# Kernel optimization log

Hardware: AMD Instinct MI355X
Metric: run time of the kernel (lower is better)

The kernel has to match this reference:

```python
import jax, jax.numpy as jnp
import numpy as np

SMOOTH_COEF = 0.025
FLOOR = 1e-06
B, T, C = 64, 4096, 128


def setup_inputs() -> dict:
    key = jax.random.key(0)
    k1, = jax.random.split(key, 1)
    inputs = jax.random.uniform(k1, (B, T, C), dtype=jnp.float32)  # nonneg spectrogram-like
    alpha = jnp.full((C,), 0.98, dtype=jnp.float32)
    delta = jnp.full((C,), 2.0, dtype=jnp.float32)
    root = jnp.full((C,), 2.0, dtype=jnp.float32)
    return {"inputs": inputs, "alpha": alpha, "delta": delta, "root": root}


def _ema(x, s):
    # m_t = s*x_t + (1-s)*m_{t-1}, with h_{-1} = x_0 => m_0 = x_0.
    # Linear recurrence via associative scan: pairs (a_t, b_t), m_t = a_t*m_{t-1} + b_t.
    Bn, Tn, Cn = x.shape
    a = jnp.full((Tn,), 1.0 - s, dtype=x.dtype).at[0].set(0.0)
    a = jnp.broadcast_to(a[None, :, None], x.shape)
    b = (s * x).at[:, 0, :].set(x[:, 0, :])

    def comb(c1, c2):
        a1, b1 = c1
        a2, b2 = c2
        return (a1 * a2, a2 * b1 + b2)

    _, m = jax.lax.associative_scan(comb, (a, b), axis=1)
    return m


def reference(inputs, alpha, delta, root):
    alpha_c = jnp.minimum(alpha, 1.0)          # [C]
    root_c = jnp.maximum(root, 1.0)            # [C]
    m = _ema(inputs, SMOOTH_COEF)              # [B,T,C] EMA smoother
    one_over_root = 1.0 / root_c
    term1 = jnp.power(FLOOR + m, alpha_c)
    term2 = jnp.power(inputs / term1 + delta, one_over_root)
    term3 = jnp.power(delta, one_over_root)
    return term2 - term3
```

## Files before the change

### kernel.cpp

```cpp
#include <hip/hip_runtime.h>


constexpr int Bn = 64, Tn = 4096, Cn = 128;
constexpr int NC = 256;
constexpr int Lc = Tn / NC;
constexpr int SUPER = 8;
constexpr int NSUP = NC / SUPER;
constexpr int SWIN = 4;
constexpr float SC  = 0.025f;
constexpr float OMS = 1.0f - SC;
constexpr float FLOORV = 1e-6f;

typedef float v4f __attribute__((ext_vector_type(4)));

__host__ __device__ constexpr float powN(float a, int n) {
    float r = 1.0f;
    for (int i = 0; i < n; ++i) r *= a;
    return r;
}
constexpr float ACH  = powN(OMS, Lc);
constexpr float ACHS = powN(OMS, Lc * SUPER);


__global__ __launch_bounds__(256) void k_partial(const float* __restrict__ x,
                                                 float* __restrict__ endv,
                                                 float* __restrict__ supv) {
    int gid   = blockIdx.x * 256 + threadIdx.x;
    int cg    = gid & 31;
    int chunk = (gid >> 5) & (NC - 1);
    int b     = gid >> 13;
    int sub   = threadIdx.x >> 5;

    const float4* xp = (const float4*)x + (size_t)(b * Tn + chunk * Lc) * (Cn / 4) + cg;

    float4 v = xp[0];
    float4 m;
    if (chunk == 0) {
        m = v;
    } else {
        m.x = SC * v.x; m.y = SC * v.y; m.z = SC * v.z; m.w = SC * v.w;
    }
#pragma unroll
    for (int t = 1; t < Lc; ++t) {
        v = xp[(size_t)t * (Cn / 4)];
        m.x = fmaf(OMS, m.x, SC * v.x);
        m.y = fmaf(OMS, m.y, SC * v.y);
        m.z = fmaf(OMS, m.z, SC * v.z);
        m.w = fmaf(OMS, m.w, SC * v.w);
    }
    ((float4*)endv)[(size_t)(b * NC + chunk) * (Cn / 4) + cg] = m;

    __shared__ float4 lds[SUPER][32];
    lds[sub][cg] = m;
    __syncthreads();
    if (threadIdx.x < 32) {
        float4 acc = lds[0][threadIdx.x];
#pragma unroll
        for (int i = 1; i < SUPER; ++i) {
            float4 e = lds[i][threadIdx.x];
            acc.x = fmaf(ACH, acc.x, e.x);
            acc.y = fmaf(ACH, acc.y, e.y);
            acc.z = fmaf(ACH, acc.z, e.z);
            acc.w = fmaf(ACH, acc.w, e.w);
        }
        ((float4*)supv)[(size_t)blockIdx.x * 32 + threadIdx.x] = acc;
    }
}

__device__ __forceinline__ float pcen_elem(float x, float m, float al, float dl,
                                           float oor, float t3) {
    float lg   = __builtin_amdgcn_logf(FLOORV + m);
    float inv1 = __builtin_amdgcn_exp2f(-al * lg);
    float base = fmaf(x, inv1, dl);
    return __builtin_amdgcn_exp2f(oor * __builtin_amdgcn_logf(base)) - t3;
}

__global__ __launch_bounds__(256) void k_final(const float* __restrict__ x,
                                               const float* __restrict__ alpha,
                                               const float* __restrict__ delta,
                                               const float* __restrict__ root,
                                               const float* __restrict__ endv,
                                               const float* __restrict__ supv,
                                               float* __restrict__ out) {
    int gid   = blockIdx.x * 256 + threadIdx.x;
    int cg    = gid & 31;
    int chunk = (gid >> 5) & (NC - 1);
    int b     = gid >> 13;

    int sc = chunk >> 3;
    const float4* Ep = (const float4*)supv + (size_t)b * NSUP * 32 + cg;
    const float4* ep = (const float4*)endv + (size_t)b * NC * (Cn / 4) + cg;

    float4 acc = {0.f, 0.f, 0.f, 0.f};
    int s0 = sc - SWIN; if (s0 < 0) s0 = 0;
#pragma unroll 4
    for (int s = s0; s < sc; ++s) {
        float4 E = Ep[(size_t)s * 32];
        acc.x = fmaf(ACHS, acc.x, E.x);
        acc.y = fmaf(ACHS, acc.y, E.y);
        acc.z = fmaf(ACHS, acc.z, E.z);
        acc.w = fmaf(ACHS, acc.w, E.w);
    }
#pragma unroll 7
    for (int j = sc * SUPER; j < chunk; ++j) {
        float4 e = ep[(size_t)j * (Cn / 4)];
        acc.x = fmaf(ACH, acc.x, e.x);
        acc.y = fmaf(ACH, acc.y, e.y);
        acc.z = fmaf(ACH, acc.z, e.z);
        acc.w = fmaf(ACH, acc.w, e.w);
    }

    int c0 = cg * 4;
    float4 al = *(const float4*)(alpha + c0);
    float4 dl = *(const float4*)(delta + c0);
    float4 rt = *(const float4*)(root + c0);
    al.x = fminf(al.x, 1.f); al.y = fminf(al.y, 1.f); al.z = fminf(al.z, 1.f); al.w = fminf(al.w, 1.f);
    rt.x = fmaxf(rt.x, 1.f); rt.y = fmaxf(rt.y, 1.f); rt.z = fmaxf(rt.z, 1.f); rt.w = fmaxf(rt.w, 1.f);
    float4 oor = {1.f / rt.x, 1.f / rt.y, 1.f / rt.z, 1.f / rt.w};
    float4 t3  = {exp2f(oor.x * log2f(dl.x)), exp2f(oor.y * log2f(dl.y)),
                  exp2f(oor.z * log2f(dl.z)), exp2f(oor.w * log2f(dl.w))};

    size_t xoff = (size_t)(b * Tn + chunk * Lc) * (Cn / 4) + cg;
    const float4* xp = (const float4*)x + xoff;
    v4f*          op = (v4f*)out + xoff;

    float4 v = xp[0];
    float4 m;
    if (chunk == 0) {
        m = v;
    } else {
        m.x = fmaf(OMS, acc.x, SC * v.x);
        m.y = fmaf(OMS, acc.y, SC * v.y);
        m.z = fmaf(OMS, acc.z, SC * v.z);
        m.w = fmaf(OMS, acc.w, SC * v.w);
    }
    v4f o;
    o.x = pcen_elem(v.x, m.x, al.x, dl.x, oor.x, t3.x);
    o.y = pcen_elem(v.y, m.y, al.y, dl.y, oor.y, t3.y);
    o.z = pcen_elem(v.z, m.z, al.z, dl.z, oor.z, t3.z);
    o.w = pcen_elem(v.w, m.w, al.w, dl.w, oor.w, t3.w);
    __builtin_nontemporal_store(o, op);

#pragma unroll
    for (int t = 1; t < Lc; ++t) {
        v = xp[(size_t)t * (Cn / 4)];
        m.x = fmaf(OMS, m.x, SC * v.x);
        m.y = fmaf(OMS, m.y, SC * v.y);
        m.z = fmaf(OMS, m.z, SC * v.z);
        m.w = fmaf(OMS, m.w, SC * v.w);
        o.x = pcen_elem(v.x, m.x, al.x, dl.x, oor.x, t3.x);
        o.y = pcen_elem(v.y, m.y, al.y, dl.y, oor.y, t3.y);
        o.z = pcen_elem(v.z, m.z, al.z, dl.z, oor.z, t3.z);
        o.w = pcen_elem(v.w, m.w, al.w, dl.w, oor.w, t3.w);
        __builtin_nontemporal_store(o, op + (size_t)t * (Cn / 4));
    }
}

extern "C" void kernel_launch(void* const* d_in, const int* in_sizes, int n_in,
                              void* d_out, int out_size, void* d_ws, size_t ws_size,
                              hipStream_t stream) {
    const float* x     = (const float*)d_in[0];
    const float* alpha = (const float*)d_in[1];
    const float* delta = (const float*)d_in[2];
    const float* root  = (const float*)d_in[3];
    float* out  = (float*)d_out;
    float* endv = (float*)d_ws;
    float* supv = (float*)d_ws + (size_t)Bn * NC * Cn;

    const int total = Bn * NC * (Cn / 4);
    k_partial<<<total / 256, 256, 0, stream>>>(x, endv, supv);
    k_final<<<total / 256, 256, 0, stream>>>(x, alpha, delta, root, endv, supv, out);
}
```

Baseline: 256.1 us.

## Fuse two-pass EMA scan into single kernel with decoupled look-back flags

Merges the partial-sum kernel and the final kernel into one. Each block keeps its 16 timesteps of input in registers, publishes its superchunk carry with an atomic release flag, and waits on the preceding superchunks' flags within a window. This avoids reading the input twice from memory, drops the endv workspace round trip, and saves a kernel launch. The costs are a memset launch, spin-waiting, higher register pressure, and a fallback path that recomputes a superchunk from x if the spin limit is hit.

```diff
diff --git a/kernel.cpp b/kernel.cpp
--- a/kernel.cpp
+++ b/kernel.cpp
@@ -2,14 +2,14 @@
 
 
 constexpr int Bn = 64, Tn = 4096, Cn = 128;
-constexpr int NC = 256;
-constexpr int Lc = Tn / NC;
+constexpr int Lc = 16;
 constexpr int SUPER = 8;
-constexpr int NSUP = NC / SUPER;
+constexpr int NSUP = 32;
 constexpr int SWIN = 4;
 constexpr float SC  = 0.025f;
 constexpr float OMS = 1.0f - SC;
 constexpr float FLOORV = 1e-6f;
+constexpr int SPIN_LIMIT = 20000;
 
 typedef float v4f __attribute__((ext_vector_type(4)));
 
@@ -20,52 +20,6 @@
 }
 constexpr float ACH  = powN(OMS, Lc);
 constexpr float ACHS = powN(OMS, Lc * SUPER);
-
-
-__global__ __launch_bounds__(256) void k_partial(const float* __restrict__ x,
-                                                 float* __restrict__ endv,
-                                                 float* __restrict__ supv) {
-    int gid   = blockIdx.x * 256 + threadIdx.x;
-    int cg    = gid & 31;
-    int chunk = (gid >> 5) & (NC - 1);
-    int b     = gid >> 13;
-    int sub   = threadIdx.x >> 5;
-
-    const float4* xp = (const float4*)x + (size_t)(b * Tn + chunk * Lc) * (Cn / 4) + cg;
-
-    float4 v = xp[0];
-    float4 m;
-    if (chunk == 0) {
-        m = v;
-    } else {
-        m.x = SC * v.x; m.y = SC * v.y; m.z = SC * v.z; m.w = SC * v.w;
-    }
-#pragma unroll
-    for (int t = 1; t < Lc; ++t) {
-        v = xp[(size_t)t * (Cn / 4)];
-        m.x = fmaf(OMS, m.x, SC * v.x);
-        m.y = fmaf(OMS, m.y, SC * v.y);
-        m.z = fmaf(OMS, m.z, SC * v.z);
-        m.w = fmaf(OMS, m.w, SC * v.w);
-    }
-    ((float4*)endv)[(size_t)(b * NC + chunk) * (Cn / 4) + cg] = m;
-
-    __shared__ float4 lds[SUPER][32];
-    lds[sub][cg] = m;
-    __syncthreads();
-    if (threadIdx.x < 32) {
-        float4 acc = lds[0][threadIdx.x];
-#pragma unroll
-        for (int i = 1; i < SUPER; ++i) {
-            float4 e = lds[i][threadIdx.x];
-            acc.x = fmaf(ACH, acc.x, e.x);
-            acc.y = fmaf(ACH, acc.y, e.y);
-            acc.z = fmaf(ACH, acc.z, e.z);
-            acc.w = fmaf(ACH, acc.w, e.w);
-        }
-        ((float4*)supv)[(size_t)blockIdx.x * 32 + threadIdx.x] = acc;
-    }
-}
 
 __device__ __forceinline__ float pcen_elem(float x, float m, float al, float dl,
                                            float oor, float t3) {
@@ -75,35 +29,118 @@
     return __builtin_amdgcn_exp2f(oor * __builtin_amdgcn_logf(base)) - t3;
 }
 
-__global__ __launch_bounds__(256) void k_final(const float* __restrict__ x,
-                                               const float* __restrict__ alpha,
-                                               const float* __restrict__ delta,
-                                               const float* __restrict__ root,
-                                               const float* __restrict__ endv,
-                                               const float* __restrict__ supv,
-                                               float* __restrict__ out) {
-    int gid   = blockIdx.x * 256 + threadIdx.x;
-    int cg    = gid & 31;
-    int chunk = (gid >> 5) & (NC - 1);
-    int b     = gid >> 13;
-
-    int sc = chunk >> 3;
-    const float4* Ep = (const float4*)supv + (size_t)b * NSUP * 32 + cg;
-    const float4* ep = (const float4*)endv + (size_t)b * NC * (Cn / 4) + cg;
+__global__ __launch_bounds__(256) void k_pcen(const float* __restrict__ x,
+                                              const float* __restrict__ alpha,
+                                              const float* __restrict__ delta,
+                                              const float* __restrict__ root,
+                                              unsigned int* __restrict__ supv,
+                                              int* __restrict__ flags,
+                                              float* __restrict__ out) {
+    const int sc  = blockIdx.x & (NSUP - 1);
+    const int b   = blockIdx.x >> 5;
+    const int cg  = threadIdx.x & 31;
+    const int sub = threadIdx.x >> 5;
+    const int chunk = sc * SUPER + sub;
+
+    const size_t xoff = (size_t)(b * Tn + chunk * Lc) * (Cn / 4) + cg;
+    const float4* xp = (const float4*)x + xoff;
+
+    float4 xr[Lc];
+#pragma unroll
+    for (int t = 0; t < Lc; ++t) xr[t] = xp[(size_t)t * (Cn / 4)];
+
+    float4 m;
+    if (chunk == 0) {
+        m = xr[0];
+    } else {
+        m.x = SC * xr[0].x; m.y = SC * xr[0].y; m.z = SC * xr[0].z; m.w = SC * xr[0].w;
+    }
+#pragma unroll
+    for (int t = 1; t < Lc; ++t) {
+        m.x = fmaf(OMS, m.x, SC * xr[t].x);
+        m.y = fmaf(OMS, m.y, SC * xr[t].y);
+        m.z = fmaf(OMS, m.z, SC * xr[t].z);
+        m.w = fmaf(OMS, m.w, SC * xr[t].w);
+    }
+
+    __shared__ float4 lds[SUPER][32];
+    lds[sub][cg] = m;
+    __syncthreads();
+
+    if (sub == SUPER - 1) {
+        float4 E = lds[0][cg];
+#pragma unroll
+        for (int i = 1; i < SUPER; ++i) {
+            float4 e = lds[i][cg];
+            E.x = fmaf(ACH, E.x, e.x);
+            E.y = fmaf(ACH, E.y, e.y);
+            E.z = fmaf(ACH, E.z, e.z);
+            E.w = fmaf(ACH, E.w, e.w);
+        }
+        unsigned int* dst = supv + ((size_t)blockIdx.x * 32 + cg) * 4;
+        __hip_atomic_store(dst + 0, __float_as_uint(E.x), __ATOMIC_RELAXED, __HIP_MEMORY_SCOPE_AGENT);
+        __hip_atomic_store(dst + 1, __float_as_uint(E.y), __ATOMIC_RELAXED, __HIP_MEMORY_SCOPE_AGENT);
+        __hip_atomic_store(dst + 2, __float_as_uint(E.z), __ATOMIC_RELAXED, __HIP_MEMORY_SCOPE_AGENT);
+        __hip_atomic_store(dst + 3, __float_as_uint(E.w), __ATOMIC_RELAXED, __HIP_MEMORY_SCOPE_AGENT);
+        __hip_atomic_fetch_add(&flags[blockIdx.x], 1, __ATOMIC_RELEASE, __HIP_MEMORY_SCOPE_AGENT);
+    }
 
     float4 acc = {0.f, 0.f, 0.f, 0.f};
     int s0 = sc - SWIN; if (s0 < 0) s0 = 0;
-#pragma unroll 4
     for (int s = s0; s < sc; ++s) {
-        float4 E = Ep[(size_t)s * 32];
+        const int fbid = (b << 5) + s;
+        int f = 0, spins = 0;
+        for (;;) {
+            f = __hip_atomic_load(&flags[fbid], __ATOMIC_ACQUIRE, __HIP_MEMORY_SCOPE_AGENT);
+            if (f >= 32) break;
+            if (++spins > SPIN_LIMIT) break;
+            __builtin_amdgcn_s_sleep(8);
+        }
+        float4 E;
+        if (f >= 32) {
+            const unsigned int* sp = supv + ((size_t)fbid * 32 + cg) * 4;
+            E.x = __uint_as_float(__hip_atomic_load(sp + 0, __ATOMIC_RELAXED, __HIP_MEMORY_SCOPE_AGENT));
+            E.y = __uint_as_float(__hip_atomic_load(sp + 1, __ATOMIC_RELAXED, __HIP_MEMORY_SCOPE_AGENT));
+            E.z = __uint_as_float(__hip_atomic_load(sp + 2, __ATOMIC_RELAXED, __HIP_MEMORY_SCOPE_AGENT));
+            E.w = __uint_as_float(__hip_atomic_load(sp + 3, __ATOMIC_RELAXED, __HIP_MEMORY_SCOPE_AGENT));
+        } else {
+            E = {0.f, 0.f, 0.f, 0.f};
+            for (int j = 0; j < SUPER; ++j) {
+                int cj = s * SUPER + j;
+                const float4* q = (const float4*)x + (size_t)(b * Tn + cj * Lc) * (Cn / 4) + cg;
+                float4 v0 = q[0];
+                float4 e;
+                if (cj == 0) {
+                    e = v0;
+                } else {
+                    e.x = SC * v0.x; e.y = SC * v0.y; e.z = SC * v0.z; e.w = SC * v0.w;
+                }
+                for (int t = 1; t < Lc; ++t) {
+                    float4 v = q[(size_t)t * (Cn / 4)];
+                    e.x = fmaf(OMS, e.x, SC * v.x);
+                    e.y = fmaf(OMS, e.y, SC * v.y);
+                    e.z = fmaf(OMS, e.z, SC * v.z);
+                    e.w = fmaf(OMS, e.w, SC * v.w);
+                }
+                if (j == 0) {
+                    E = e;
+                } else {
+                    E.x = fmaf(ACH, E.x, e.x);
+                    E.y = fmaf(ACH, E.y, e.y);
+                    E.z = fmaf(ACH, E.z, e.z);
+                    E.w = fmaf(ACH, E.w, e.w);
+                }
+            }
+        }
         acc.x = fmaf(ACHS, acc.x, E.x);
         acc.y = fmaf(ACHS, acc.y, E.y);
         acc.z = fmaf(ACHS, acc.z, E.z);
         acc.w = fmaf(ACHS, acc.w, E.w);
     }
+
 #pragma unroll 7
-    for (int j = sc * SUPER; j < chunk; ++j) {
-        float4 e = ep[(size_t)j * (Cn / 4)];
+    for (int j = 0; j < sub; ++j) {
+        float4 e = lds[j][cg];
         acc.x = fmaf(ACH, acc.x, e.x);
         acc.y = fmaf(ACH, acc.y, e.y);
         acc.z = fmaf(ACH, acc.z, e.z);
@@ -120,38 +157,31 @@
     float4 t3  = {exp2f(oor.x * log2f(dl.x)), exp2f(oor.y * log2f(dl.y)),
                   exp2f(oor.z * log2f(dl.z)), exp2f(oor.w * log2f(dl.w))};
 
-    size_t xoff = (size_t)(b * Tn + chunk * Lc) * (Cn / 4) + cg;
-    const float4* xp = (const float4*)x + xoff;
-    v4f*          op = (v4f*)out + xoff;
-
-    float4 v = xp[0];
-    float4 m;
+    v4f* op = (v4f*)out + xoff;
     if (chunk == 0) {
-        m = v;
+        m = xr[0];
     } else {
-        m.x = fmaf(OMS, acc.x, SC * v.x);
-        m.y = fmaf(OMS, acc.y, SC * v.y);
-        m.z = fmaf(OMS, acc.z, SC * v.z);
-        m.w = fmaf(OMS, acc.w, SC * v.w);
+        m.x = fmaf(OMS, acc.x, SC * xr[0].x);
+        m.y = fmaf(OMS, acc.y, SC * xr[0].y);
+        m.z = fmaf(OMS, acc.z, SC * xr[0].z);
+        m.w = fmaf(OMS, acc.w, SC * xr[0].w);
     }
     v4f o;
-    o.x = pcen_elem(v.x, m.x, al.x, dl.x, oor.x, t3.x);
-    o.y = pcen_elem(v.y, m.y, al.y, dl.y, oor.y, t3.y);
-    o.z = pcen_elem(v.z, m.z, al.z, dl.z, oor.z, t3.z);
-    o.w = pcen_elem(v.w, m.w, al.w, dl.w, oor.w, t3.w);
+    o.x = pcen_elem(xr[0].x, m.x, al.x, dl.x, oor.x, t3.x);
+    o.y = pcen_elem(xr[0].y, m.y, al.y, dl.y, oor.y, t3.y);
+    o.z = pcen_elem(xr[0].z, m.z, al.z, dl.z, oor.z, t3.z);
+    o.w = pcen_elem(xr[0].w, m.w, al.w, dl.w, oor.w, t3.w);
     __builtin_nontemporal_store(o, op);
-
 #pragma unroll
     for (int t = 1; t < Lc; ++t) {
-        v = xp[(size_t)t * (Cn / 4)];
-        m.x = fmaf(OMS, m.x, SC * v.x);
-        m.y = fmaf(OMS, m.y, SC * v.y);
-        m.z = fmaf(OMS, m.z, SC * v.z);
-        m.w = fmaf(OMS, m.w, SC * v.w);
-        o.x = pcen_elem(v.x, m.x, al.x, dl.x, oor.x, t3.x);
-        o.y = pcen_elem(v.y, m.y, al.y, dl.y, oor.y, t3.y);
-        o.z = pcen_elem(v.z, m.z, al.z, dl.z, oor.z, t3.z);
-        o.w = pcen_elem(v.w, m.w, al.w, dl.w, oor.w, t3.w);
+        m.x = fmaf(OMS, m.x, SC * xr[t].x);
+        m.y = fmaf(OMS, m.y, SC * xr[t].y);
+        m.z = fmaf(OMS, m.z, SC * xr[t].z);
+        m.w = fmaf(OMS, m.w, SC * xr[t].w);
+        o.x = pcen_elem(xr[t].x, m.x, al.x, dl.x, oor.x, t3.x);
+        o.y = pcen_elem(xr[t].y, m.y, al.y, dl.y, oor.y, t3.y);
+        o.z = pcen_elem(xr[t].z, m.z, al.z, dl.z, oor.z, t3.z);
+        o.w = pcen_elem(xr[t].w, m.w, al.w, dl.w, oor.w, t3.w);
         __builtin_nontemporal_store(o, op + (size_t)t * (Cn / 4));
     }
 }
@@ -163,11 +193,12 @@
     const float* alpha = (const float*)d_in[1];
     const float* delta = (const float*)d_in[2];
     const float* root  = (const float*)d_in[3];
-    float* out  = (float*)d_out;
-    float* endv = (float*)d_ws;
-    float* supv = (float*)d_ws + (size_t)Bn * NC * Cn;
-
-    const int total = Bn * NC * (Cn / 4);
-    k_partial<<<total / 256, 256, 0, stream>>>(x, endv, supv);
-    k_final<<<total / 256, 256, 0, stream>>>(x, alpha, delta, root, endv, supv, out);
-}
+    float* out = (float*)d_out;
+
+    unsigned int* supv = (unsigned int*)d_ws;
+    int* flags = (int*)((char*)d_ws + (size_t)Bn * NSUP * Cn * 4);
+
+    hipMemsetAsync(flags, 0, Bn * NSUP * sizeof(int), stream);
+    const int nblocks = Bn * NSUP;
+    k_pcen<<<nblocks, 256, 0, stream>>>(x, alpha, delta, root, supv, flags, out);
+}
```

Result: slower. 568.4 us (+121.9%).
